# Kernel tuning notes

Hardware: AMD Instinct MI355X
Metric: run time of the kernel (lower is better)

The kernel has to match this reference:

```python
import jax, jax.numpy as jnp
import numpy as np

TW = 25          # time_window
H = 128          # hidden_features
NL = 6           # hidden_layer
N = 8192         # batch*n_nodes
E = 131072       # edges (avg degree 16)
EDGE_DIM = 51    # 50 (u diff) + 1 (pos_x diff)
LEM_IN = 4       # pos_x, u_ch0, u_ch1, ts
PDE_L = 16.0
PDE_TMAX = 4.0
PDE_DT = 0.04
NEG_SLOPE = 0.2  # PyG GATConv leaky_relu slope


def swish(x):
    return x * jax.nn.sigmoid(x)


def setup_inputs() -> dict:
    key = jax.random.key(0)
    ks = jax.random.split(key, 32)
    def p(k, shape, s=0.05):
        return jax.random.normal(k, shape, jnp.float32) * s
    inp = {}
    inp['u'] = jax.random.normal(ks[0], (N, 2 * TW), jnp.float32)
    inp['pos'] = jax.random.uniform(ks[1], (N, 2), jnp.float32)
    inp['edge_index'] = jax.random.randint(ks[2], (2, E), 0, N)
    # LEM cell params (inp2hid: 4H, hid2hid: 3H, transform_z: H)
    inp['lem_inp_w'] = p(ks[3], (4 * H, LEM_IN)); inp['lem_inp_b'] = jnp.zeros(4 * H, jnp.float32)
    inp['lem_hid_w'] = p(ks[4], (3 * H, H));      inp['lem_hid_b'] = jnp.zeros(3 * H, jnp.float32)
    inp['lem_z_w'] = p(ks[5], (H, H));            inp['lem_z_b'] = jnp.zeros(H, jnp.float32)
    # lemoutput_mlp
    inp['mlp1_w'] = p(ks[6], (H, H)); inp['mlp1_b'] = jnp.zeros(H, jnp.float32)
    inp['mlp2_w'] = p(ks[7], (H, H)); inp['mlp2_b'] = jnp.zeros(H, jnp.float32)
    # main GAT layers (stacked over NL)
    inp['gnn_lin_w'] = p(ks[8], (NL, H, H)); inp['gnn_edge_w'] = p(ks[9], (NL, H, EDGE_DIM))
    inp['gnn_att_src'] = p(ks[10], (NL, H)); inp['gnn_att_dst'] = p(ks[11], (NL, H))
    inp['gnn_att_edge'] = p(ks[12], (NL, H)); inp['gnn_bias'] = jnp.zeros((NL, H), jnp.float32)
    # gate GAT layers
    inp['gate_lin_w'] = p(ks[13], (NL, H, H)); inp['gate_edge_w'] = p(ks[14], (NL, H, EDGE_DIM))
    inp['gate_att_src'] = p(ks[15], (NL, H)); inp['gate_att_dst'] = p(ks[16], (NL, H))
    inp['gate_att_edge'] = p(ks[17], (NL, H)); inp['gate_bias'] = jnp.zeros((NL, H), jnp.float32)
    # double_mlp + conv1d decoder (time_window==25 branch)
    inp['dbl_w'] = p(ks[18], (2 * H, H)); inp['dbl_b'] = jnp.zeros(2 * H, jnp.float32)
    inp['conv1_w'] = p(ks[19], (8, 2, 16)); inp['conv1_b'] = jnp.zeros(8, jnp.float32)
    inp['conv2_w'] = p(ks[20], (2, 8, 14)); inp['conv2_b'] = jnp.zeros(2, jnp.float32)
    return inp


def _gat(x, src, dst, edge_attr, lin_w, edge_w, a_src, a_dst, a_edge, bias):
    """Single-head GATConv with edge features (PyG semantics, aggregate at dst)."""
    xt = x @ lin_w.T                      # [N,H]
    et = edge_attr @ edge_w.T             # [E,H]
    logits = jax.nn.leaky_relu((xt @ a_src)[src] + (xt @ a_dst)[dst] + et @ a_edge, NEG_SLOPE)
    amax = jax.ops.segment_max(logits, dst, num_segments=N)
    amax = jnp.where(jnp.isfinite(amax), amax, 0.0)
    ex = jnp.exp(logits - amax[dst])
    denom = jax.ops.segment_sum(ex, dst, num_segments=N)
    w = ex / (denom[dst] + 1e-16)         # edge softmax over incoming edges
    out = jax.ops.segment_sum(w[:, None] * xt[src], dst, num_segments=N)
    return out + bias


def _forward(u, pos, lem_inp_w, lem_inp_b, lem_hid_w, lem_hid_b, lem_z_w, lem_z_b,
             mlp1_w, mlp1_b, mlp2_w, mlp2_b,
             gnn_lin_w, gnn_edge_w, gnn_att_src, gnn_att_dst, gnn_att_edge, gnn_bias,
             gate_lin_w, gate_edge_w, gate_att_src, gate_att_dst, gate_att_edge, gate_bias,
             dbl_w, dbl_b, conv1_w, conv1_b, conv2_w, conv2_b, edge_index):
    pos_x = pos[:, 1:2] / PDE_L    # [N,1]
    pos_t = pos[:, 0:1] / PDE_TMAX # [N,1]
    dt = jnp.cumsum(jnp.full((TW,), PDE_DT, jnp.float32))  # [TW]
    ts = pos_t + dt[None, :]       # [N,TW]
    # LEM input: [TW, N, 4] = (pos_x, u channel 0, u channel 1, ts)
    lem_x = jnp.concatenate([
        jnp.broadcast_to(pos_x[None, :, :], (TW, N, 1)),
        u[:, :TW].T[:, :, None],
        u[:, TW:].T[:, :, None],
        ts.T[:, :, None],
    ], axis=-1)

    def cell(carry, xt):
        y, z = carry
        ii = xt @ lem_inp_w.T + lem_inp_b   # [N,4H]
        hh = y @ lem_hid_w.T + lem_hid_b    # [N,3H]
        i1, i2, i3, i4 = jnp.split(ii, 4, axis=-1)
        h1, h2, h3 = jnp.split(hh, 3, axis=-1)
        ms_dt_bar = jax.nn.sigmoid(i1 + h1)
        ms_dt = jax.nn.sigmoid(i2 + h2)
        z = (1.0 - ms_dt) * z + ms_dt * jnp.tanh(i3 + h3)
        y = (1.0 - ms_dt_bar) * y + ms_dt_bar * jnp.tanh(z @ lem_z_w.T + lem_z_b + i4)
        return (y, z), None

    y0 = jnp.zeros((N, H), u.dtype)
    (y, _), _ = jax.lax.scan(cell, (y0, y0), lem_x)
    h = swish(y @ mlp1_w.T + mlp1_b)
    h = swish(h @ mlp2_w.T + mlp2_b)

    src, dst = edge_index[0], edge_index[1]
    edge_attr = jnp.concatenate([u[src] - u[dst], pos_x[src] - pos_x[dst]], axis=-1)  # [E,51]

    for i in range(NL):
        tau = jax.nn.sigmoid(_gat(h, src, dst, edge_attr, gate_lin_w[i], gate_edge_w[i],
                                  gate_att_src[i], gate_att_dst[i], gate_att_edge[i], gate_bias[i]))
        msg = swish(_gat(h, src, dst, edge_attr, gnn_lin_w[i], gnn_edge_w[i],
                         gnn_att_src[i], gnn_att_dst[i], gnn_att_edge[i], gnn_bias[i]))
        h = (1.0 - tau) * h + tau * msg

    h2 = swish(h @ dbl_w.T + dbl_b).reshape(N, 2, H)  # [N,2,128]
    dn = ('NCH', 'OIH', 'NCH')
    d = jax.lax.conv_general_dilated(h2, conv1_w, (3,), 'VALID', dimension_numbers=dn)
    d = swish(d + conv1_b[None, :, None])              # [N,8,38]
    d = jax.lax.conv_general_dilated(d, conv2_w, (1,), 'VALID', dimension_numbers=dn)
    d = d + conv2_b[None, :, None]                     # [N,2,25]
    out = u.reshape(N, 2, TW) + dt[None, None, :] * d
    return out.reshape(N, 2 * TW)


def reference(u, pos, edge_index, lem_inp_w, lem_inp_b, lem_hid_w, lem_hid_b, lem_z_w, lem_z_b,
              mlp1_w, mlp1_b, mlp2_w, mlp2_b,
              gnn_lin_w, gnn_edge_w, gnn_att_src, gnn_att_dst, gnn_att_edge, gnn_bias,
              gate_lin_w, gate_edge_w, gate_att_src, gate_att_dst, gate_att_edge, gate_bias,
              dbl_w, dbl_b, conv1_w, conv1_b, conv2_w, conv2_b):
    return _forward(u, pos, lem_inp_w, lem_inp_b, lem_hid_w, lem_hid_b, lem_z_w, lem_z_b,
                    mlp1_w, mlp1_b, mlp2_w, mlp2_b,
                    gnn_lin_w, gnn_edge_w, gnn_att_src, gnn_att_dst, gnn_att_edge, gnn_bias,
                    gate_lin_w, gate_edge_w, gate_att_src, gate_att_dst, gate_att_edge, gate_bias,
                    dbl_w, dbl_b, conv1_w, conv1_b, conv2_w, conv2_b, edge_index)
```

## Files before the change

### kernel.cpp

```cpp
#include <hip/hip_runtime.h>

#define N_NODES 8192
#define N_EDGES 131072

using short8 = __attribute__((ext_vector_type(8))) short;
using f32x4  = __attribute__((ext_vector_type(4))) float;

__device__ __forceinline__ float rcpf(float x){ return __builtin_amdgcn_rcpf(x); }
__device__ __forceinline__ float sigm(float x){ return rcpf(1.0f+__expf(-x)); }
__device__ __forceinline__ float ftanh(float x){ float e=__expf(2.0f*x); return (e-1.0f)*rcpf(e+1.0f); }
__device__ __forceinline__ float swishf(float x){ return x*sigm(x); }
__device__ __forceinline__ float leaky(float x){ return x>=0.0f? x : 0.2f*x; }
__device__ __forceinline__ float dot4(float4 a, float4 b){ return a.x*b.x+a.y*b.y+a.z*b.z+a.w*b.w; }
__device__ __forceinline__ short f2bf(float x){
  unsigned u=__float_as_uint(x);
  unsigned r=(u + 0x7fffu + ((u>>16)&1u))>>16;
  return (short)r;
}
__device__ __forceinline__ int pack2bf(float a, float b){
  return (int)(((unsigned)(unsigned short)f2bf(a)) | (((unsigned)(unsigned short)f2bf(b))<<16));
}

__device__ __forceinline__ float wave_rmax(float v){
  #pragma unroll
  for(int m=32;m;m>>=1) v=fmaxf(v,__shfl_xor(v,m));
  return v;
}
__device__ __forceinline__ float wave_rsum(float v){
  #pragma unroll
  for(int m=32;m;m>>=1) v+=__shfl_xor(v,m);
  return v;
}

__global__ __launch_bounds__(256) void hist_kernel(const int* __restrict__ dst, int* __restrict__ cnt){
  int e=blockIdx.x*256+threadIdx.x;
  if(e<N_EDGES) atomicAdd(&cnt[dst[e]],1);
}

__global__ __launch_bounds__(1024) void scan_kernel(const int* __restrict__ cnt, int* __restrict__ rowptr, int* __restrict__ cursor){
  __shared__ int sums[1024];
  int t=threadIdx.x; int base=t*8;
  int local[8]; int s=0;
  #pragma unroll
  for(int i=0;i<8;++i){ local[i]=s; s+=cnt[base+i]; }
  sums[t]=s; __syncthreads();
  for(int off=1;off<1024;off<<=1){
    int v=(t>=off)?sums[t-off]:0;
    __syncthreads();
    sums[t]+=v;
    __syncthreads();
  }
  int offset=(t>0)?sums[t-1]:0;
  #pragma unroll
  for(int i=0;i<8;++i){ int v=offset+local[i]; rowptr[base+i]=v; cursor[base+i]=v; }
  if(t==1023) rowptr[N_NODES]=sums[1023];
}

__global__ __launch_bounds__(256) void scatter_kernel(const int* __restrict__ src, const int* __restrict__ dst,
                                                      int* __restrict__ cursor, int* __restrict__ csr_src){
  int e=blockIdx.x*256+threadIdx.x;
  if(e<N_EDGES){
    int slot=atomicAdd(&cursor[dst[e]],1);
    csr_src[slot]=src[e];
  }
}

__global__ __launch_bounds__(256) void prep_bf16_kernel(
    const float* __restrict__ lem_hid_w, const float* __restrict__ lem_z_w,
    const float* __restrict__ mlp1_w, const float* __restrict__ mlp2_w,
    const float* __restrict__ gate_lin_w, const float* __restrict__ gnn_lin_w,
    short* __restrict__ whb, short* __restrict__ wzb, short* __restrict__ w1b,
    short* __restrict__ w2b, short* __restrict__ wlin16)
{
  int i=blockIdx.x*256+threadIdx.x;
  if(i<49152){ whb[i]=f2bf(lem_hid_w[i]); return; }
  if(i<65536){ int k=i-49152; wzb[k]=f2bf(lem_z_w[k]); return; }
  if(i<81920){ int k=i-65536; w1b[k]=f2bf(mlp1_w[k]); return; }
  if(i<98304){ int k=i-81920; w2b[k]=f2bf(mlp2_w[k]); return; }
  int k=i-98304;
  int l=k>>15, which=(k>>14)&1, r=k&16383;
  const float* s = which? gnn_lin_w + l*16384 + r : gate_lin_w + l*16384 + r;
  wlin16[k]=f2bf(*s);
}

__global__ __launch_bounds__(256) void we_kernel(const float* __restrict__ gate_ew, const float* __restrict__ gnn_ew,
                                                 const float* __restrict__ gate_ae, const float* __restrict__ gnn_ae,
                                                 float* __restrict__ we){
  int idx=blockIdx.x*256+threadIdx.x;
  if(idx>=12*51) return;
  int g=idx/51, k=idx%51, l=g>>1;
  const float* ew = (g&1)? gnn_ew + l*128*51 : gate_ew + l*128*51;
  const float* ae = (g&1)? gnn_ae + l*128    : gate_ae + l*128;
  float s=0.f;
  for(int f=0;f<128;++f) s+=ew[f*51+k]*ae[f];
  we[idx]=s;
}

__global__ __launch_bounds__(128) void gsc_kernel(const float* __restrict__ u, const float* __restrict__ pos,
                                                  const float* __restrict__ we, float* __restrict__ gsc){
  int n=blockIdx.x*128+threadIdx.x;
  float uv[50];
  #pragma unroll
  for(int k=0;k<50;++k) uv[k]=u[n*50+k];
  float px=pos[n*2+1]*(1.0f/16.0f);
  for(int g=0;g<12;++g){
    const float* w=we+g*51;
    float s=w[50]*px;
    #pragma unroll
    for(int k=0;k<50;++k) s+=w[k]*uv[k];
    gsc[g*N_NODES+n]=s;
  }
}

__device__ __forceinline__ void transform_phase(
    int tid, int n0,
    const short* __restrict__ h16, short* __restrict__ xts,
    float* __restrict__ ssred, float* __restrict__ sdred,
    const short* __restrict__ wl,
    const float* __restrict__ a_sg, const float* __restrict__ a_dg,
    const float* __restrict__ a_sm, const float* __restrict__ a_dm,
    const float* __restrict__ gsc_g, const float* __restrict__ gsc_m,
    short* __restrict__ xt_out, float* __restrict__ ss_out, float* __restrict__ sd_out)
{
  const int lane=tid&63, w=tid>>6;
  const int cg=w&1, ch=w>>1;
  const int r16=lane&15, kq=lane>>4;
  __syncthreads();
  short8 afr[4];
  #pragma unroll
  for(int kk=0;kk<4;++kk)
    afr[kk]=*(const short8*)&h16[r16*128 + ((kk*32+kq*8) ^ ((r16&7)<<3))];
  const short* wb = wl + cg*16384;
  const float* as_ = cg? a_sm : a_sg;
  const float* ad_ = cg? a_dm : a_dg;
  float ssp[4]={0,0,0,0}, sdp[4]={0,0,0,0};
  #pragma unroll
  for(int ci=0;ci<2;++ci){
    int c0=(ch*2+ci)*16;
    f32x4 acc={0.f,0.f,0.f,0.f};
    #pragma unroll
    for(int kk=0;kk<4;++kk){
      short8 b=*(const short8*)(wb + (c0+r16)*128 + kk*32 + kq*8);
      acc=__builtin_amdgcn_mfma_f32_16x16x32_bf16(afr[kk],b,acc,0,0,0);
    }
    float av=as_[c0+r16], dv=ad_[c0+r16];
    #pragma unroll
    for(int r=0;r<4;++r){
      ssp[r]+=acc[r]*av; sdp[r]+=acc[r]*dv;
      xts[(kq*4+r)*256 + cg*128 + c0 + r16]=f2bf(acc[r]);
    }
  }
  #pragma unroll
  for(int m=1;m<16;m<<=1){
    #pragma unroll
    for(int r=0;r<4;++r){ ssp[r]+=__shfl_xor(ssp[r],m); sdp[r]+=__shfl_xor(sdp[r],m); }
  }
  if(r16==0){
    #pragma unroll
    for(int r=0;r<4;++r){ ssred[w*16+kq*4+r]=ssp[r]; sdred[w*16+kq*4+r]=sdp[r]; }
  }
  __syncthreads();
  if(tid<32){
    int node=tid&15, cg2=tid>>4;
    float sv=0.f, dv=0.f;
    #pragma unroll
    for(int c2=0;c2<4;++c2){ sv+=ssred[(c2*2+cg2)*16+node]; dv+=sdred[(c2*2+cg2)*16+node]; }
    float gv=(cg2? gsc_m:gsc_g)[n0+node];
    ss_out[2*(n0+node)+cg2]=sv+gv;
    sd_out[2*(n0+node)+cg2]=dv-gv;
  }
  {
    const short8* sp=(const short8*)xts;
    short8* dp=(short8*)(xt_out + (size_t)n0*256);
    dp[tid]=sp[tid];
  }
}

__device__ __forceinline__ float4 aggregate_node(
    int n, int lane,
    const int* __restrict__ rowptr, const int* __restrict__ csr_src,
    const short* __restrict__ xt_in, const float* __restrict__ ss_in, const float* __restrict__ sd_in,
    const float* __restrict__ bias_g, const float* __restrict__ bias_m,
    const float* __restrict__ h)
{
  const int s0=rowptr[n], deg=rowptr[n+1]-s0;
  const float2 sdv=*(const float2*)(sd_in+2*n);
  const float bg=sdv.x, bm=sdv.y;
  float mg=-1e30f, mm=-1e30f;
  for(int c=0;c<deg;c+=64){
    int i=c+lane;
    if(i<deg){
      int s=csr_src[s0+i];
      float2 ssv=*(const float2*)(ss_in+2*s);
      mg=fmaxf(mg,leaky(ssv.x+bg)); mm=fmaxf(mm,leaky(ssv.y+bm));
    }
  }
  mg=wave_rmax(mg); mm=wave_rmax(mm);
  float dg=0.f,dm=0.f, acc0=0.f,acc1=0.f,acc2=0.f,acc3=0.f;
  for(int c=0;c<deg;c+=64){
    int i=c+lane, s=0; float eg=0.f, em=0.f;
    if(i<deg){
      s=csr_src[s0+i];
      float2 ssv=*(const float2*)(ss_in+2*s);
      eg=__expf(leaky(ssv.x+bg)-mg); em=__expf(leaky(ssv.y+bm)-mm);
      dg+=eg; dm+=em;
    }
    int cntc=min(64,deg-c);
    for(int cb=0;cb<cntc;cb+=8){
      int sj[8]; float wj[8];
      #pragma unroll
      for(int jj=0;jj<8;++jj){
        int idx=cb+jj;
        int sv=__shfl(s,idx);
        float wg=__shfl(eg,idx), wm=__shfl(em,idx);
        sj[jj]=sv;
        wj[jj]= lane<32? wg : wm;
      }
      uint2 rows[8];
      #pragma unroll
      for(int jj=0;jj<8;++jj)
        rows[jj]=*(const uint2*)(xt_in + (size_t)sj[jj]*256 + 4*lane);
      #pragma unroll
      for(int jj=0;jj<8;++jj){
        float wv=wj[jj];
        unsigned p0=rows[jj].x, p1=rows[jj].y;
        acc0+=wv*__uint_as_float(p0<<16);
        acc1+=wv*__uint_as_float(p0&0xffff0000u);
        acc2+=wv*__uint_as_float(p1<<16);
        acc3+=wv*__uint_as_float(p1&0xffff0000u);
      }
    }
  }
  dg=wave_rsum(dg); dm=wave_rsum(dm);
  float rr = lane<32? rcpf(dg+1e-16f) : rcpf(dm+1e-16f);
  const float* bp = lane<32? bias_g+4*lane : bias_m+4*(lane-32);
  float4 bv=*(const float4*)bp;
  float o0=acc0*rr+bv.x, o1=acc1*rr+bv.y, o2=acc2*rr+bv.z, o3=acc3*rr+bv.w;
  float s0_=sigm(o0), s1_=sigm(o1), s2_=sigm(o2), s3_=sigm(o3);
  float v0=lane<32? s0_:o0*s0_;
  float v1=lane<32? s1_:o1*s1_;
  float v2=lane<32? s2_:o2*s2_;
  float v3=lane<32? s3_:o3*s3_;
  float m0=__shfl_xor(v0,32), m1=__shfl_xor(v1,32), m2=__shfl_xor(v2,32), m3=__shfl_xor(v3,32);
  float4 r;
  if(lane<32){
    float4 hv=*(const float4*)(h + (size_t)n*128 + 4*lane);
    r.x=(1.0f-v0)*hv.x+v0*m0;
    r.y=(1.0f-v1)*hv.y+v1*m1;
    r.z=(1.0f-v2)*hv.z+v2*m2;
    r.w=(1.0f-v3)*hv.w+v3*m3;
  } else { r.x=r.y=r.z=r.w=0.f; }
  return r;
}

__global__ __launch_bounds__(512,2) void lem_t0_kernel(
    const float* __restrict__ u, const float* __restrict__ pos,
    const float* __restrict__ Wi, const float* __restrict__ bi,
    const short* __restrict__ whb, const float* __restrict__ bh,
    const short* __restrict__ wzb, const float* __restrict__ bz,
    const short* __restrict__ w1b, const float* __restrict__ b1,
    const short* __restrict__ w2b, const float* __restrict__ b2,
    float* __restrict__ hout,
    const short* __restrict__ wl,
    const float* __restrict__ a_sg, const float* __restrict__ a_dg,
    const float* __restrict__ a_sm, const float* __restrict__ a_dm,
    const float* __restrict__ gsc_g, const float* __restrict__ gsc_m,
    short* __restrict__ xt_out, float* __restrict__ ss_out, float* __restrict__ sd_out)
{
  __shared__ short y16[16*128];
  __shared__ short z16[16*128];
  __shared__ float u_s[16*50];
  __shared__ float hstg[16*132];
  __shared__ short h16[16*128];
  __shared__ short xts[16*256];
  __shared__ float ssred[128], sdred[128];

  const int tid=threadIdx.x, lane=tid&63, w=tid>>6;
  const int node=lane&15, q=lane>>4;
  const int n7=node&7;
  const int n0=blockIdx.x*16;

  for(int i=tid;i<16*50;i+=512) u_s[i]=u[n0*50+i];
  for(int i=tid;i<16*64;i+=512) ((int*)y16)[i]=0;

  const float px = pos[(n0+node)*2+1]*(1.0f/16.0f);
  const float pt = pos[(n0+node)*2+0]*0.25f;

  float cbase[4][4], cslope[4][4], ca[4][4], cb[4][4];
  #pragma unroll
  for(int gg=0; gg<4; ++gg){
    #pragma unroll
    for(int r=0;r<4;++r){
      int fr = w*16+q*4+r;
      int row = gg*128+fr;
      float4 wi = *(const float4*)(Wi+4*row);
      float bb = bi[row] + ((gg<3)? bh[row] : bz[fr]);
      cbase[gg][r] = bb + wi.x*px + wi.w*pt;
      cslope[gg][r]= wi.w*0.04f;
      ca[gg][r]=wi.y; cb[gg][r]=wi.z;
    }
  }

  short8 whf[3][4];
  #pragma unroll
  for(int gg=0;gg<3;++gg)
    #pragma unroll
    for(int kk=0;kk<4;++kk)
      whf[gg][kk]=*(const short8*)(whb + (gg*128 + w*16 + node)*128 + kk*32 + q*8);
  short8 wzf[4];
  #pragma unroll
  for(int kk=0;kk<4;++kk)
    wzf[kk]=*(const short8*)(wzb + (w*16 + node)*128 + kk*32 + q*8);

  float yreg[4]={0.f,0.f,0.f,0.f}, zreg[4]={0.f,0.f,0.f,0.f};
  float msb[4], i4s[4];
  const int wrslot = (w*16+q*4) ^ (n7<<3);
  __syncthreads();

  for(int t=0;t<25;++t){
    f32x4 h1a={0.f,0.f,0.f,0.f}, h2a=h1a, h3a=h1a;
    #pragma unroll
    for(int kk=0;kk<4;++kk){
      short8 yb=*(const short8*)&y16[node*128 + ((kk*32 + q*8) ^ (n7<<3))];
      h1a=__builtin_amdgcn_mfma_f32_16x16x32_bf16(whf[0][kk],yb,h1a,0,0,0);
      h2a=__builtin_amdgcn_mfma_f32_16x16x32_bf16(whf[1][kk],yb,h2a,0,0,0);
      h3a=__builtin_amdgcn_mfma_f32_16x16x32_bf16(whf[2][kk],yb,h3a,0,0,0);
    }
    const float u0=u_s[node*50+t], u1=u_s[node*50+25+t];
    const float tf=(float)(t+1);
    #pragma unroll
    for(int r=0;r<4;++r){
      float i1=cbase[0][r]+cslope[0][r]*tf+ca[0][r]*u0+cb[0][r]*u1;
      float i2=cbase[1][r]+cslope[1][r]*tf+ca[1][r]*u0+cb[1][r]*u1;
      float i3=cbase[2][r]+cslope[2][r]*tf+ca[2][r]*u0+cb[2][r]*u1;
      i4s[r]  =cbase[3][r]+cslope[3][r]*tf+ca[3][r]*u0+cb[3][r]*u1;
      msb[r]=sigm(i1+h1a[r]);
      float ms=sigm(i2+h2a[r]);
      zreg[r]=(1.0f-ms)*zreg[r]+ms*ftanh(i3+h3a[r]);
    }
    { int2 zz; zz.x=pack2bf(zreg[0],zreg[1]); zz.y=pack2bf(zreg[2],zreg[3]);
      *(int2*)&z16[node*128 + wrslot]=zz; }
    __syncthreads();
    f32x4 zw={0.f,0.f,0.f,0.f};
    #pragma unroll
    for(int kk=0;kk<4;++kk){
      short8 zb=*(const short8*)&z16[node*128 + ((kk*32 + q*8) ^ (n7<<3))];
      zw=__builtin_amdgcn_mfma_f32_16x16x32_bf16(wzf[kk],zb,zw,0,0,0);
    }
    #pragma unroll
    for(int r=0;r<4;++r)
      yreg[r]=(1.0f-msb[r])*yreg[r]+msb[r]*ftanh(zw[r]+i4s[r]);
    { int2 yy; yy.x=pack2bf(yreg[0],yreg[1]); yy.y=pack2bf(yreg[2],yreg[3]);
      *(int2*)&y16[node*128 + wrslot]=yy; }
    __syncthreads();
  }

  {
    short8 w1f[4];
    #pragma unroll
    for(int kk=0;kk<4;++kk)
      w1f[kk]=*(const short8*)(w1b + (w*16 + node)*128 + kk*32 + q*8);
    float4 b1v=*(const float4*)(b1 + w*16 + q*4);
    f32x4 a={0.f,0.f,0.f,0.f};
    #pragma unroll
    for(int kk=0;kk<4;++kk){
      short8 yb=*(const short8*)&y16[node*128 + ((kk*32 + q*8) ^ (n7<<3))];
      a=__builtin_amdgcn_mfma_f32_16x16x32_bf16(w1f[kk],yb,a,0,0,0);
    }
    float t0=swishf(a[0]+b1v.x), t1=swishf(a[1]+b1v.y);
    float t2=swishf(a[2]+b1v.z), t3=swishf(a[3]+b1v.w);
    int2 zz; zz.x=pack2bf(t0,t1); zz.y=pack2bf(t2,t3);
    *(int2*)&z16[node*128 + wrslot]=zz;
  }
  __syncthreads();
  {
    short8 w2f[4];
    #pragma unroll
    for(int kk=0;kk<4;++kk)
      w2f[kk]=*(const short8*)(w2b + (w*16 + node)*128 + kk*32 + q*8);
    float4 b2v=*(const float4*)(b2 + w*16 + q*4);
    f32x4 a={0.f,0.f,0.f,0.f};
    #pragma unroll
    for(int kk=0;kk<4;++kk){
      short8 zb=*(const short8*)&z16[node*128 + ((kk*32 + q*8) ^ (n7<<3))];
      a=__builtin_amdgcn_mfma_f32_16x16x32_bf16(w2f[kk],zb,a,0,0,0);
    }
    float h0=swishf(a[0]+b2v.x), h1=swishf(a[1]+b2v.y);
    float h2=swishf(a[2]+b2v.z), h3=swishf(a[3]+b2v.w);
    hstg[node*132 + w*16+q*4+0]=h0;
    hstg[node*132 + w*16+q*4+1]=h1;
    hstg[node*132 + w*16+q*4+2]=h2;
    hstg[node*132 + w*16+q*4+3]=h3;
    int2 hb; hb.x=pack2bf(h0,h1); hb.y=pack2bf(h2,h3);
    *(int2*)&h16[node*128 + wrslot]=hb;
  }
  __syncthreads();
  for(int i=tid;i<16*128;i+=512){
    int nn=i>>7, ff=i&127;
    hout[(n0+nn)*128+ff]=hstg[nn*132+ff];
  }
  transform_phase(tid,n0,h16,xts,ssred,sdred,wl,a_sg,a_dg,a_sm,a_dm,gsc_g,gsc_m,xt_out,ss_out,sd_out);
}

__global__ __launch_bounds__(512,2) void gat_fused_kernel(
    const int* __restrict__ rowptr, const int* __restrict__ csr_src,
    const short* __restrict__ xt_in, const float* __restrict__ ss_in, const float* __restrict__ sd_in,
    const float* __restrict__ bias_g, const float* __restrict__ bias_m,
    float* __restrict__ h,
    const short* __restrict__ wl,
    const float* __restrict__ a_sg, const float* __restrict__ a_dg,
    const float* __restrict__ a_sm, const float* __restrict__ a_dm,
    const float* __restrict__ gsc_g, const float* __restrict__ gsc_m,
    short* __restrict__ xt_out, float* __restrict__ ss_out, float* __restrict__ sd_out)
{
  __shared__ short h16[16*128];
  __shared__ short xts[16*256];
  __shared__ float ssred[128], sdred[128];
  const int tid=threadIdx.x, lane=tid&63, w=tid>>6;
  const int n0=blockIdx.x*16;
  #pragma unroll
  for(int which=0;which<2;++which){
    int row=w*2+which, n=n0+row;
    float4 hv=aggregate_node(n,lane,rowptr,csr_src,xt_in,ss_in,sd_in,bias_g,bias_m,h);
    if(lane<32){
      *(float4*)(h+(size_t)n*128+4*lane)=hv;
      int2 hb; hb.x=pack2bf(hv.x,hv.y); hb.y=pack2bf(hv.z,hv.w);
      *(int2*)&h16[row*128 + ((4*lane) ^ ((row&7)<<3))]=hb;
    }
  }
  transform_phase(tid,n0,h16,xts,ssred,sdred,wl,a_sg,a_dg,a_sm,a_dm,gsc_g,gsc_m,xt_out,ss_out,sd_out);
}

__global__ __launch_bounds__(512,2) void gat_last_decoder_kernel(
    const int* __restrict__ rowptr, const int* __restrict__ csr_src,
    const short* __restrict__ xt_in, const float* __restrict__ ss_in, const float* __restrict__ sd_in,
    const float* __restrict__ bias_g, const float* __restrict__ bias_m,
    const float* __restrict__ h, const float* __restrict__ u,
    const float* __restrict__ Wd, const float* __restrict__ bd,
    const float* __restrict__ w1, const float* __restrict__ b1,
    const float* __restrict__ w2, const float* __restrict__ b2,
    float* __restrict__ out)
{
  __shared__ float hdec[16*128];
  __shared__ float h2[16][2][128];
  __shared__ float c1[16][8][38];
  __shared__ float w1s[256], w2s[224], b1s[8], b2s[2];
  const int tid=threadIdx.x, lane=tid&63, w=tid>>6;
  const int n0=blockIdx.x*16;
  if(tid<256) w1s[tid]=w1[tid];
  else if(tid<480) w2s[tid-256]=w2[tid-256];
  else if(tid<488) b1s[tid-480]=b1[tid-480];
  else if(tid<490) b2s[tid-488]=b2[tid-488];
  #pragma unroll
  for(int which=0;which<2;++which){
    int row=w*2+which, n=n0+row;
    float4 hv=aggregate_node(n,lane,rowptr,csr_src,xt_in,ss_in,sd_in,bias_g,bias_m,h);
    if(lane<32) *(float4*)&hdec[row*128+4*lane]=hv;
  }
  __syncthreads();
  {
    int o=tid&255, grp=tid>>8;
    const float4* wp=(const float4*)(Wd + o*128);
    float acc[8];
    #pragma unroll
    for(int n=0;n<8;++n) acc[n]=0.f;
    for(int k=0;k<32;++k){
      float4 wv=wp[k];
      #pragma unroll
      for(int n=0;n<8;++n){ float4 hval=*(const float4*)&hdec[(grp*8+n)*128+k*4]; acc[n]+=dot4(wv,hval); }
    }
    float bdv=bd[o];
    int chn=o>>7, p=o&127;
    #pragma unroll
    for(int n=0;n<8;++n) h2[grp*8+n][chn][p]=swishf(acc[n]+bdv);
  }
  __syncthreads();
  for(int idx=tid; idx<16*8*38; idx+=512){
    int n=idx/(8*38); int r=idx%(8*38); int oc=r/38, p=r%38;
    float acc=b1s[oc];
    const float* ww=&w1s[oc*32];
    #pragma unroll
    for(int ic=0;ic<2;++ic)
      #pragma unroll
      for(int k=0;k<16;++k) acc+=ww[ic*16+k]*h2[n][ic][3*p+k];
    c1[n][oc][p]=swishf(acc);
  }
  __syncthreads();
  for(int idx=tid; idx<16*2*25; idx+=512){
    int n=idx/50; int r=idx%50; int oc=r/25, p=r%25;
    float acc=b2s[oc];
    const float* ww=&w2s[oc*112];
    #pragma unroll
    for(int ic=0;ic<8;++ic)
      #pragma unroll
      for(int k=0;k<14;++k) acc+=ww[ic*14+k]*c1[n][ic][p+k];
    int col=oc*25+p;
    out[(n0+n)*50+col]=u[(n0+n)*50+col]+0.04f*(float)(p+1)*acc;
  }
}

extern "C" void kernel_launch(void* const* d_in, const int* in_sizes, int n_in,
                              void* d_out, int out_size, void* d_ws, size_t ws_size,
                              hipStream_t stream)
{
  const float* u          =(const float*)d_in[0];
  const float* pos        =(const float*)d_in[1];
  const int*   ei         =(const int*)d_in[2];
  const float* lem_inp_w  =(const float*)d_in[3];
  const float* lem_inp_b  =(const float*)d_in[4];
  const float* lem_hid_w  =(const float*)d_in[5];
  const float* lem_hid_b  =(const float*)d_in[6];
  const float* lem_z_w    =(const float*)d_in[7];
  const float* lem_z_b    =(const float*)d_in[8];
  const float* mlp1_w     =(const float*)d_in[9];
  const float* mlp1_b     =(const float*)d_in[10];
  const float* mlp2_w     =(const float*)d_in[11];
  const float* mlp2_b     =(const float*)d_in[12];
  const float* gnn_lin_w  =(const float*)d_in[13];
  const float* gnn_edge_w =(const float*)d_in[14];
  const float* gnn_att_src=(const float*)d_in[15];
  const float* gnn_att_dst=(const float*)d_in[16];
  const float* gnn_att_edge=(const float*)d_in[17];
  const float* gnn_bias   =(const float*)d_in[18];
  const float* gate_lin_w =(const float*)d_in[19];
  const float* gate_edge_w=(const float*)d_in[20];
  const float* gate_att_src=(const float*)d_in[21];
  const float* gate_att_dst=(const float*)d_in[22];
  const float* gate_att_edge=(const float*)d_in[23];
  const float* gate_bias  =(const float*)d_in[24];
  const float* dbl_w      =(const float*)d_in[25];
  const float* dbl_b      =(const float*)d_in[26];
  const float* conv1_w    =(const float*)d_in[27];
  const float* conv1_b    =(const float*)d_in[28];
  const float* conv2_w    =(const float*)d_in[29];
  const float* conv2_b    =(const float*)d_in[30];
  float* out=(float*)d_out;

  char* ws=(char*)d_ws;
  size_t off=0;
  auto alloc=[&](size_t bytes)->char*{ char* p=ws+off; off+=(bytes+255)&~(size_t)255; return p; };
  float* h    =(float*)alloc((size_t)N_NODES*128*4);
  short* xtA  =(short*)alloc((size_t)N_NODES*256*2);
  short* xtB  =(short*)alloc((size_t)N_NODES*256*2);
  float* ssA  =(float*)alloc((size_t)N_NODES*2*4);
  float* ssB  =(float*)alloc((size_t)N_NODES*2*4);
  float* sdA  =(float*)alloc((size_t)N_NODES*2*4);
  float* sdB  =(float*)alloc((size_t)N_NODES*2*4);
  float* gsc  =(float*)alloc((size_t)12*N_NODES*4);
  float* wearr=(float*)alloc(12*51*4);
  int* cnt    =(int*)alloc(N_NODES*4);
  int* rowptr =(int*)alloc((N_NODES+8)*4);
  int* cursor =(int*)alloc(N_NODES*4);
  int* csrsrc =(int*)alloc((size_t)N_EDGES*4);
  short* whb  =(short*)alloc(384*128*2);
  short* wzb  =(short*)alloc(128*128*2);
  short* w1b  =(short*)alloc(128*128*2);
  short* w2b  =(short*)alloc(128*128*2);
  short* wlin16=(short*)alloc((size_t)6*2*128*128*2);

  const int* src=ei;
  const int* dst=ei+N_EDGES;

  hipMemsetAsync(cnt,0,N_NODES*4,stream);
  hist_kernel<<<N_EDGES/256,256,0,stream>>>(dst,cnt);
  scan_kernel<<<1,1024,0,stream>>>(cnt,rowptr,cursor);
  scatter_kernel<<<N_EDGES/256,256,0,stream>>>(src,dst,cursor,csrsrc);
  prep_bf16_kernel<<<(294912+255)/256,256,0,stream>>>(lem_hid_w,lem_z_w,mlp1_w,mlp2_w,
                                                      gate_lin_w,gnn_lin_w,
                                                      whb,wzb,w1b,w2b,wlin16);
  we_kernel<<<3,256,0,stream>>>(gate_edge_w,gnn_edge_w,gate_att_edge,gnn_att_edge,wearr);
  gsc_kernel<<<N_NODES/128,128,0,stream>>>(u,pos,wearr,gsc);

  short* xtbuf[2]={xtA,xtB};
  float* ssbuf[2]={ssA,ssB};
  float* sdbuf[2]={sdA,sdB};

  lem_t0_kernel<<<N_NODES/16,512,0,stream>>>(u,pos,lem_inp_w,lem_inp_b,whb,lem_hid_b,
      wzb,lem_z_b,w1b,mlp1_b,w2b,mlp2_b,h,
      wlin16,
      gate_att_src, gate_att_dst, gnn_att_src, gnn_att_dst,
      gsc, gsc+(size_t)N_NODES,
      xtbuf[0], ssbuf[0], sdbuf[0]);

  for(int l=0;l<5;++l){
    int in=l&1, o2=(l+1)&1;
    gat_fused_kernel<<<N_NODES/16,512,0,stream>>>(rowptr,csrsrc,
      xtbuf[in],ssbuf[in],sdbuf[in],
      gate_bias+l*128, gnn_bias+l*128, h,
      wlin16+(size_t)(l+1)*2*16384,
      gate_att_src+(l+1)*128, gate_att_dst+(l+1)*128,
      gnn_att_src+(l+1)*128, gnn_att_dst+(l+1)*128,
      gsc+(size_t)(2*(l+1))*N_NODES, gsc+(size_t)(2*(l+1)+1)*N_NODES,
      xtbuf[o2], ssbuf[o2], sdbuf[o2]);
  }

  gat_last_decoder_kernel<<<N_NODES/16,512,0,stream>>>(rowptr,csrsrc,
      xtbuf[1],ssbuf[1],sdbuf[1],
      gate_bias+5*128, gnn_bias+5*128, h, u,
      dbl_w, dbl_b, conv1_w, conv1_b, conv2_w, conv2_b, out);
}
```

Measured before the change: 376.1 us.

## Process two node tiles per LEM block, drop softmax max pass, fuse weight prep kernels

```diff
diff --git a/kernel.cpp b/kernel.cpp
--- a/kernel.cpp
+++ b/kernel.cpp
@@ -17,15 +17,10 @@
   unsigned r=(u + 0x7fffu + ((u>>16)&1u))>>16;
   return (short)r;
 }
-__device__ __forceinline__ int pack2bf(float a, float b){
-  return (int)(((unsigned)(unsigned short)f2bf(a)) | (((unsigned)(unsigned short)f2bf(b))<<16));
-}
-
-__device__ __forceinline__ float wave_rmax(float v){
-  #pragma unroll
-  for(int m=32;m;m>>=1) v=fmaxf(v,__shfl_xor(v,m));
-  return v;
-}
+__device__ __forceinline__ int cvtpk(float a, float b){
+  int r; asm("v_cvt_pk_bf16_f32 %0, %1, %2" : "=v"(r) : "v"(a), "v"(b)); return r;
+}
+
 __device__ __forceinline__ float wave_rsum(float v){
   #pragma unroll
   for(int m=32;m;m>>=1) v+=__shfl_xor(v,m);
@@ -69,24 +64,24 @@
     const float* __restrict__ lem_hid_w, const float* __restrict__ lem_z_w,
     const float* __restrict__ mlp1_w, const float* __restrict__ mlp2_w,
     const float* __restrict__ gate_lin_w, const float* __restrict__ gnn_lin_w,
+    const float* __restrict__ gate_ew, const float* __restrict__ gnn_ew,
+    const float* __restrict__ gate_ae, const float* __restrict__ gnn_ae,
     short* __restrict__ whb, short* __restrict__ wzb, short* __restrict__ w1b,
-    short* __restrict__ w2b, short* __restrict__ wlin16)
+    short* __restrict__ w2b, short* __restrict__ wlin16, float* __restrict__ we)
 {
   int i=blockIdx.x*256+threadIdx.x;
   if(i<49152){ whb[i]=f2bf(lem_hid_w[i]); return; }
   if(i<65536){ int k=i-49152; wzb[k]=f2bf(lem_z_w[k]); return; }
   if(i<81920){ int k=i-65536; w1b[k]=f2bf(mlp1_w[k]); return; }
   if(i<98304){ int k=i-81920; w2b[k]=f2bf(mlp2_w[k]); return; }
-  int k=i-98304;
-  int l=k>>15, which=(k>>14)&1, r=k&16383;
-  const float* s = which? gnn_lin_w + l*16384 + r : gate_lin_w + l*16384 + r;
-  wlin16[k]=f2bf(*s);
-}
-
-__global__ __launch_bounds__(256) void we_kernel(const float* __restrict__ gate_ew, const float* __restrict__ gnn_ew,
-                                                 const float* __restrict__ gate_ae, const float* __restrict__ gnn_ae,
-                                                 float* __restrict__ we){
-  int idx=blockIdx.x*256+threadIdx.x;
+  if(i<294912){
+    int k=i-98304;
+    int l=k>>15, which=(k>>14)&1, r=k&16383;
+    const float* s = which? gnn_lin_w + l*16384 + r : gate_lin_w + l*16384 + r;
+    wlin16[k]=f2bf(*s);
+    return;
+  }
+  int idx=i-294912;
   if(idx>=12*51) return;
   int g=idx/51, k=idx%51, l=g>>1;
   const float* ew = (g&1)? gnn_ew + l*128*51 : gate_ew + l*128*51;
@@ -186,23 +181,14 @@
   const int s0=rowptr[n], deg=rowptr[n+1]-s0;
   const float2 sdv=*(const float2*)(sd_in+2*n);
   const float bg=sdv.x, bm=sdv.y;
-  float mg=-1e30f, mm=-1e30f;
-  for(int c=0;c<deg;c+=64){
-    int i=c+lane;
-    if(i<deg){
-      int s=csr_src[s0+i];
-      float2 ssv=*(const float2*)(ss_in+2*s);
-      mg=fmaxf(mg,leaky(ssv.x+bg)); mm=fmaxf(mm,leaky(ssv.y+bm));
-    }
-  }
-  mg=wave_rmax(mg); mm=wave_rmax(mm);
   float dg=0.f,dm=0.f, acc0=0.f,acc1=0.f,acc2=0.f,acc3=0.f;
   for(int c=0;c<deg;c+=64){
     int i=c+lane, s=0; float eg=0.f, em=0.f;
     if(i<deg){
       s=csr_src[s0+i];
       float2 ssv=*(const float2*)(ss_in+2*s);
-      eg=__expf(leaky(ssv.x+bg)-mg); em=__expf(leaky(ssv.y+bm)-mm);
+      eg=__expf(fminf(leaky(ssv.x+bg),60.f));
+      em=__expf(fminf(leaky(ssv.y+bm),60.f));
       dg+=eg; dm+=em;
     }
     int cntc=min(64,deg-c);
@@ -210,9 +196,8 @@
       int sj[8]; float wj[8];
       #pragma unroll
       for(int jj=0;jj<8;++jj){
-        int idx=cb+jj;
-        int sv=__shfl(s,idx);
-        float wg=__shfl(eg,idx), wm=__shfl(em,idx);
+        int sv=__shfl(s,cb+jj);
+        float wg=__shfl(eg,cb+jj), wm=__shfl(em,cb+jj);
         sj[jj]=sv;
         wj[jj]= lane<32? wg : wm;
       }
@@ -267,10 +252,9 @@
     const float* __restrict__ gsc_g, const float* __restrict__ gsc_m,
     short* __restrict__ xt_out, float* __restrict__ ss_out, float* __restrict__ sd_out)
 {
-  __shared__ short y16[16*128];
-  __shared__ short z16[16*128];
-  __shared__ float u_s[16*50];
-  __shared__ float hstg[16*132];
+  __shared__ short y16[2][16*128];
+  __shared__ short z16[2][16*128];
+  __shared__ float u_s[32*50];
   __shared__ short h16[16*128];
   __shared__ short xts[16*256];
   __shared__ float ssred[128], sdred[128];
@@ -278,15 +262,15 @@
   const int tid=threadIdx.x, lane=tid&63, w=tid>>6;
   const int node=lane&15, q=lane>>4;
   const int n7=node&7;
-  const int n0=blockIdx.x*16;
-
-  for(int i=tid;i<16*50;i+=512) u_s[i]=u[n0*50+i];
-  for(int i=tid;i<16*64;i+=512) ((int*)y16)[i]=0;
-
-  const float px = pos[(n0+node)*2+1]*(1.0f/16.0f);
-  const float pt = pos[(n0+node)*2+0]*0.25f;
-
-  float cbase[4][4], cslope[4][4], ca[4][4], cb[4][4];
+  const int n0=blockIdx.x*32;
+
+  for(int i=tid;i<32*50;i+=512) u_s[i]=u[n0*50+i];
+  for(int i=tid;i<2*16*64;i+=512) ((int*)y16)[i]=0;
+
+  const float px0=pos[(n0+node)*2+1]*(1.0f/16.0f),    pt0=pos[(n0+node)*2+0]*0.25f;
+  const float px1=pos[(n0+16+node)*2+1]*(1.0f/16.0f), pt1=pos[(n0+16+node)*2+0]*0.25f;
+
+  float bb[4][4], wix[4][4], wiw[4][4], wiy[4][4], wiz[4][4];
   #pragma unroll
   for(int gg=0; gg<4; ++gg){
     #pragma unroll
@@ -294,10 +278,8 @@
       int fr = w*16+q*4+r;
       int row = gg*128+fr;
       float4 wi = *(const float4*)(Wi+4*row);
-      float bb = bi[row] + ((gg<3)? bh[row] : bz[fr]);
-      cbase[gg][r] = bb + wi.x*px + wi.w*pt;
-      cslope[gg][r]= wi.w*0.04f;
-      ca[gg][r]=wi.y; cb[gg][r]=wi.z;
+      bb[gg][r] = bi[row] + ((gg<3)? bh[row] : bz[fr]);
+      wix[gg][r]=wi.x; wiw[gg][r]=wi.w; wiy[gg][r]=wi.y; wiz[gg][r]=wi.z;
     }
   }
 
@@ -312,94 +294,134 @@
   for(int kk=0;kk<4;++kk)
     wzf[kk]=*(const short8*)(wzb + (w*16 + node)*128 + kk*32 + q*8);
 
-  float yreg[4]={0.f,0.f,0.f,0.f}, zreg[4]={0.f,0.f,0.f,0.f};
-  float msb[4], i4s[4];
+  float yr0[4]={0.f,0.f,0.f,0.f}, zr0[4]={0.f,0.f,0.f,0.f};
+  float yr1[4]={0.f,0.f,0.f,0.f}, zr1[4]={0.f,0.f,0.f,0.f};
+  float msb0[4], i4s0[4], msb1[4], i4s1[4];
   const int wrslot = (w*16+q*4) ^ (n7<<3);
+  const int rdbase = n7<<3;
   __syncthreads();
 
   for(int t=0;t<25;++t){
-    f32x4 h1a={0.f,0.f,0.f,0.f}, h2a=h1a, h3a=h1a;
-    #pragma unroll
-    for(int kk=0;kk<4;++kk){
-      short8 yb=*(const short8*)&y16[node*128 + ((kk*32 + q*8) ^ (n7<<3))];
-      h1a=__builtin_amdgcn_mfma_f32_16x16x32_bf16(whf[0][kk],yb,h1a,0,0,0);
-      h2a=__builtin_amdgcn_mfma_f32_16x16x32_bf16(whf[1][kk],yb,h2a,0,0,0);
-      h3a=__builtin_amdgcn_mfma_f32_16x16x32_bf16(whf[2][kk],yb,h3a,0,0,0);
-    }
-    const float u0=u_s[node*50+t], u1=u_s[node*50+25+t];
     const float tf=(float)(t+1);
-    #pragma unroll
-    for(int r=0;r<4;++r){
-      float i1=cbase[0][r]+cslope[0][r]*tf+ca[0][r]*u0+cb[0][r]*u1;
-      float i2=cbase[1][r]+cslope[1][r]*tf+ca[1][r]*u0+cb[1][r]*u1;
-      float i3=cbase[2][r]+cslope[2][r]*tf+ca[2][r]*u0+cb[2][r]*u1;
-      i4s[r]  =cbase[3][r]+cslope[3][r]*tf+ca[3][r]*u0+cb[3][r]*u1;
-      msb[r]=sigm(i1+h1a[r]);
-      float ms=sigm(i2+h2a[r]);
-      zreg[r]=(1.0f-ms)*zreg[r]+ms*ftanh(i3+h3a[r]);
-    }
-    { int2 zz; zz.x=pack2bf(zreg[0],zreg[1]); zz.y=pack2bf(zreg[2],zreg[3]);
-      *(int2*)&z16[node*128 + wrslot]=zz; }
+    {
+      f32x4 h1a={0.f,0.f,0.f,0.f}, h2a=h1a, h3a=h1a;
+      #pragma unroll
+      for(int kk=0;kk<4;++kk){
+        short8 yb=*(const short8*)&y16[0][node*128 + ((kk*32 + q*8) ^ rdbase)];
+        h1a=__builtin_amdgcn_mfma_f32_16x16x32_bf16(whf[0][kk],yb,h1a,0,0,0);
+        h2a=__builtin_amdgcn_mfma_f32_16x16x32_bf16(whf[1][kk],yb,h2a,0,0,0);
+        h3a=__builtin_amdgcn_mfma_f32_16x16x32_bf16(whf[2][kk],yb,h3a,0,0,0);
+      }
+      const float u0=u_s[node*50+t], u1=u_s[node*50+25+t];
+      const float ts=pt0+0.04f*tf;
+      #pragma unroll
+      for(int r=0;r<4;++r){
+        float i1=bb[0][r]+wix[0][r]*px0+wiw[0][r]*ts+wiy[0][r]*u0+wiz[0][r]*u1;
+        float i2=bb[1][r]+wix[1][r]*px0+wiw[1][r]*ts+wiy[1][r]*u0+wiz[1][r]*u1;
+        float i3=bb[2][r]+wix[2][r]*px0+wiw[2][r]*ts+wiy[2][r]*u0+wiz[2][r]*u1;
+        i4s0[r] =bb[3][r]+wix[3][r]*px0+wiw[3][r]*ts+wiy[3][r]*u0+wiz[3][r]*u1;
+        msb0[r]=sigm(i1+h1a[r]);
+        float ms=sigm(i2+h2a[r]);
+        zr0[r]=(1.0f-ms)*zr0[r]+ms*ftanh(i3+h3a[r]);
+      }
+      int2 zz; zz.x=cvtpk(zr0[0],zr0[1]); zz.y=cvtpk(zr0[2],zr0[3]);
+      *(int2*)&z16[0][node*128 + wrslot]=zz;
+    }
+    {
+      f32x4 h1a={0.f,0.f,0.f,0.f}, h2a=h1a, h3a=h1a;
+      #pragma unroll
+      for(int kk=0;kk<4;++kk){
+        short8 yb=*(const short8*)&y16[1][node*128 + ((kk*32 + q*8) ^ rdbase)];
+        h1a=__builtin_amdgcn_mfma_f32_16x16x32_bf16(whf[0][kk],yb,h1a,0,0,0);
+        h2a=__builtin_amdgcn_mfma_f32_16x16x32_bf16(whf[1][kk],yb,h2a,0,0,0);
+        h3a=__builtin_amdgcn_mfma_f32_16x16x32_bf16(whf[2][kk],yb,h3a,0,0,0);
+      }
+      const float u0=u_s[(16+node)*50+t], u1=u_s[(16+node)*50+25+t];
+      const float ts=pt1+0.04f*tf;
+      #pragma unroll
+      for(int r=0;r<4;++r){
+        float i1=bb[0][r]+wix[0][r]*px1+wiw[0][r]*ts+wiy[0][r]*u0+wiz[0][r]*u1;
+        float i2=bb[1][r]+wix[1][r]*px1+wiw[1][r]*ts+wiy[1][r]*u0+wiz[1][r]*u1;
+        float i3=bb[2][r]+wix[2][r]*px1+wiw[2][r]*ts+wiy[2][r]*u0+wiz[2][r]*u1;
+        i4s1[r] =bb[3][r]+wix[3][r]*px1+wiw[3][r]*ts+wiy[3][r]*u0+wiz[3][r]*u1;
+        msb1[r]=sigm(i1+h1a[r]);
+        float ms=sigm(i2+h2a[r]);
+        zr1[r]=(1.0f-ms)*zr1[r]+ms*ftanh(i3+h3a[r]);
+      }
+      int2 zz; zz.x=cvtpk(zr1[0],zr1[1]); zz.y=cvtpk(zr1[2],zr1[3]);
+      *(int2*)&z16[1][node*128 + wrslot]=zz;
+    }
     __syncthreads();
-    f32x4 zw={0.f,0.f,0.f,0.f};
-    #pragma unroll
-    for(int kk=0;kk<4;++kk){
-      short8 zb=*(const short8*)&z16[node*128 + ((kk*32 + q*8) ^ (n7<<3))];
-      zw=__builtin_amdgcn_mfma_f32_16x16x32_bf16(wzf[kk],zb,zw,0,0,0);
-    }
-    #pragma unroll
-    for(int r=0;r<4;++r)
-      yreg[r]=(1.0f-msb[r])*yreg[r]+msb[r]*ftanh(zw[r]+i4s[r]);
-    { int2 yy; yy.x=pack2bf(yreg[0],yreg[1]); yy.y=pack2bf(yreg[2],yreg[3]);
-      *(int2*)&y16[node*128 + wrslot]=yy; }
+    {
+      f32x4 zw={0.f,0.f,0.f,0.f};
+      #pragma unroll
+      for(int kk=0;kk<4;++kk){
+        short8 zb=*(const short8*)&z16[0][node*128 + ((kk*32 + q*8) ^ rdbase)];
+        zw=__builtin_amdgcn_mfma_f32_16x16x32_bf16(wzf[kk],zb,zw,0,0,0);
+      }
+      #pragma unroll
+      for(int r=0;r<4;++r)
+        yr0[r]=(1.0f-msb0[r])*yr0[r]+msb0[r]*ftanh(zw[r]+i4s0[r]);
+      int2 yy; yy.x=cvtpk(yr0[0],yr0[1]); yy.y=cvtpk(yr0[2],yr0[3]);
+      *(int2*)&y16[0][node*128 + wrslot]=yy;
+    }
+    {
+      f32x4 zw={0.f,0.f,0.f,0.f};
+      #pragma unroll
+      for(int kk=0;kk<4;++kk){
+        short8 zb=*(const short8*)&z16[1][node*128 + ((kk*32 + q*8) ^ rdbase)];
+        zw=__builtin_amdgcn_mfma_f32_16x16x32_bf16(wzf[kk],zb,zw,0,0,0);
+      }
+      #pragma unroll
+      for(int r=0;r<4;++r)
+        yr1[r]=(1.0f-msb1[r])*yr1[r]+msb1[r]*ftanh(zw[r]+i4s1[r]);
+      int2 yy; yy.x=cvtpk(yr1[0],yr1[1]); yy.y=cvtpk(yr1[2],yr1[3]);
+      *(int2*)&y16[1][node*128 + wrslot]=yy;
+    }
     __syncthreads();
   }
 
-  {
-    short8 w1f[4];
-    #pragma unroll
-    for(int kk=0;kk<4;++kk)
-      w1f[kk]=*(const short8*)(w1b + (w*16 + node)*128 + kk*32 + q*8);
-    float4 b1v=*(const float4*)(b1 + w*16 + q*4);
-    f32x4 a={0.f,0.f,0.f,0.f};
-    #pragma unroll
-    for(int kk=0;kk<4;++kk){
-      short8 yb=*(const short8*)&y16[node*128 + ((kk*32 + q*8) ^ (n7<<3))];
-      a=__builtin_amdgcn_mfma_f32_16x16x32_bf16(w1f[kk],yb,a,0,0,0);
-    }
-    float t0=swishf(a[0]+b1v.x), t1=swishf(a[1]+b1v.y);
-    float t2=swishf(a[2]+b1v.z), t3=swishf(a[3]+b1v.w);
-    int2 zz; zz.x=pack2bf(t0,t1); zz.y=pack2bf(t2,t3);
-    *(int2*)&z16[node*128 + wrslot]=zz;
-  }
-  __syncthreads();
-  {
-    short8 w2f[4];
-    #pragma unroll
-    for(int kk=0;kk<4;++kk)
-      w2f[kk]=*(const short8*)(w2b + (w*16 + node)*128 + kk*32 + q*8);
-    float4 b2v=*(const float4*)(b2 + w*16 + q*4);
-    f32x4 a={0.f,0.f,0.f,0.f};
-    #pragma unroll
-    for(int kk=0;kk<4;++kk){
-      short8 zb=*(const short8*)&z16[node*128 + ((kk*32 + q*8) ^ (n7<<3))];
-      a=__builtin_amdgcn_mfma_f32_16x16x32_bf16(w2f[kk],zb,a,0,0,0);
-    }
-    float h0=swishf(a[0]+b2v.x), h1=swishf(a[1]+b2v.y);
-    float h2=swishf(a[2]+b2v.z), h3=swishf(a[3]+b2v.w);
-    hstg[node*132 + w*16+q*4+0]=h0;
-    hstg[node*132 + w*16+q*4+1]=h1;
-    hstg[node*132 + w*16+q*4+2]=h2;
-    hstg[node*132 + w*16+q*4+3]=h3;
-    int2 hb; hb.x=pack2bf(h0,h1); hb.y=pack2bf(h2,h3);
-    *(int2*)&h16[node*128 + wrslot]=hb;
-  }
-  __syncthreads();
-  for(int i=tid;i<16*128;i+=512){
-    int nn=i>>7, ff=i&127;
-    hout[(n0+nn)*128+ff]=hstg[nn*132+ff];
-  }
-  transform_phase(tid,n0,h16,xts,ssred,sdred,wl,a_sg,a_dg,a_sm,a_dm,gsc_g,gsc_m,xt_out,ss_out,sd_out);
+  #pragma unroll
+  for(int nt=0;nt<2;++nt){
+    {
+      short8 w1f[4];
+      #pragma unroll
+      for(int kk=0;kk<4;++kk)
+        w1f[kk]=*(const short8*)(w1b + (w*16 + node)*128 + kk*32 + q*8);
+      float4 b1v=*(const float4*)(b1 + w*16 + q*4);
+      f32x4 a={0.f,0.f,0.f,0.f};
+      #pragma unroll
+      for(int kk=0;kk<4;++kk){
+        short8 yb=*(const short8*)&y16[nt][node*128 + ((kk*32 + q*8) ^ rdbase)];
+        a=__builtin_amdgcn_mfma_f32_16x16x32_bf16(w1f[kk],yb,a,0,0,0);
+      }
+      float t0=swishf(a[0]+b1v.x), t1=swishf(a[1]+b1v.y);
+      float t2=swishf(a[2]+b1v.z), t3=swishf(a[3]+b1v.w);
+      int2 zz; zz.x=cvtpk(t0,t1); zz.y=cvtpk(t2,t3);
+      *(int2*)&z16[nt][node*128 + wrslot]=zz;
+    }
+    __syncthreads();
+    {
+      short8 w2f[4];
+      #pragma unroll
+      for(int kk=0;kk<4;++kk)
+        w2f[kk]=*(const short8*)(w2b + (w*16 + node)*128 + kk*32 + q*8);
+      float4 b2v=*(const float4*)(b2 + w*16 + q*4);
+      f32x4 a={0.f,0.f,0.f,0.f};
+      #pragma unroll
+      for(int kk=0;kk<4;++kk){
+        short8 zb=*(const short8*)&z16[nt][node*128 + ((kk*32 + q*8) ^ rdbase)];
+        a=__builtin_amdgcn_mfma_f32_16x16x32_bf16(w2f[kk],zb,a,0,0,0);
+      }
+      float h0=swishf(a[0]+b2v.x), h1=swishf(a[1]+b2v.y);
+      float h2=swishf(a[2]+b2v.z), h3=swishf(a[3]+b2v.w);
+      float4 hv; hv.x=h0; hv.y=h1; hv.z=h2; hv.w=h3;
+      *(float4*)(hout + (size_t)(n0+nt*16+node)*128 + w*16+q*4)=hv;
+      int2 hb; hb.x=cvtpk(h0,h1); hb.y=cvtpk(h2,h3);
+      *(int2*)&h16[node*128 + wrslot]=hb;
+    }
+    transform_phase(tid,n0+nt*16,h16,xts,ssred,sdred,wl,a_sg,a_dg,a_sm,a_dm,gsc_g,gsc_m,xt_out,ss_out,sd_out);
+  }
 }
 
 __global__ __launch_bounds__(512,2) void gat_fused_kernel(
@@ -424,7 +446,7 @@
     float4 hv=aggregate_node(n,lane,rowptr,csr_src,xt_in,ss_in,sd_in,bias_g,bias_m,h);
     if(lane<32){
       *(float4*)(h+(size_t)n*128+4*lane)=hv;
-      int2 hb; hb.x=pack2bf(hv.x,hv.y); hb.y=pack2bf(hv.z,hv.w);
+      int2 hb; hb.x=cvtpk(hv.x,hv.y); hb.y=cvtpk(hv.z,hv.w);
       *(int2*)&h16[row*128 + ((4*lane) ^ ((row&7)<<3))]=hb;
     }
   }
@@ -565,17 +587,17 @@
   hist_kernel<<<N_EDGES/256,256,0,stream>>>(dst,cnt);
   scan_kernel<<<1,1024,0,stream>>>(cnt,rowptr,cursor);
   scatter_kernel<<<N_EDGES/256,256,0,stream>>>(src,dst,cursor,csrsrc);
-  prep_bf16_kernel<<<(294912+255)/256,256,0,stream>>>(lem_hid_w,lem_z_w,mlp1_w,mlp2_w,
+  prep_bf16_kernel<<<(294912+612+255)/256,256,0,stream>>>(lem_hid_w,lem_z_w,mlp1_w,mlp2_w,
                                                       gate_lin_w,gnn_lin_w,
-                                                      whb,wzb,w1b,w2b,wlin16);
-  we_kernel<<<3,256,0,stream>>>(gate_edge_w,gnn_edge_w,gate_att_edge,gnn_att_edge,wearr);
+                                                      gate_edge_w,gnn_edge_w,gate_att_edge,gnn_att_edge,
+                                                      whb,wzb,w1b,w2b,wlin16,wearr);
   gsc_kernel<<<N_NODES/128,128,0,stream>>>(u,pos,wearr,gsc);
 
   short* xtbuf[2]={xtA,xtB};
   float* ssbuf[2]={ssA,ssB};
   float* sdbuf[2]={sdA,sdB};
 
-  lem_t0_kernel<<<N_NODES/16,512,0,stream>>>(u,pos,lem_inp_w,lem_inp_b,whb,lem_hid_b,
+  lem_t0_kernel<<<N_NODES/32,512,0,stream>>>(u,pos,lem_inp_w,lem_inp_b,whb,lem_hid_b,
       wzb,lem_z_b,w1b,mlp1_b,w2b,mlp2_b,h,
       wlin16,
       gate_att_src, gate_att_dst, gnn_att_src, gnn_att_dst,
```

Result: faster. 358.4 us (-4.7%).
